# Kernel tuning notes

Measured on AMD Instinct MI355X. Metric: run time of the kernel, lower is better.

Reference implementation:

```python
import jax, jax.numpy as jnp
import numpy as np
from jax import lax

V_TH = 1.0
ALPHA = 2.0  # ATan surrogate alpha
EPS = 1e-5

@jax.custom_vjp
def heaviside(x):
    return (x >= 0).astype(x.dtype)

def _hv_fwd(x):
    return (x >= 0).astype(x.dtype), x

def _hv_bwd(x, g):
    # ATan surrogate: alpha/2 / (1 + (pi/2 * alpha * x)^2)
    return (g * (ALPHA / 2.0) / (1.0 + (jnp.pi / 2.0 * ALPHA * x) ** 2),)

heaviside.defvjp(_hv_fwd, _hv_bwd)

def if_multistep(x_seq):
    # IF neuron, v_threshold=1.0, v_reset=0.0 (hard reset), over leading time dim
    def step(v, x):
        h = v + x
        s = heaviside(h - V_TH)
        v_new = h * (1.0 - s)  # hard reset to 0
        return v_new, s
    _, spikes = lax.scan(step, jnp.zeros_like(x_seq[0]), x_seq)
    return spikes

def conv2d(x, w):
    return lax.conv_general_dilated(x, w, (1, 1), 'SAME',
                                    dimension_numbers=('NCHW', 'OIHW', 'NCHW'))

def bn(x, g, b, m, v):
    inv = g / jnp.sqrt(v + EPS)
    return x * inv[None, :, None, None] + (b - m * inv)[None, :, None, None]

def maxpool2(x):  # [N,C,H,W] -> [N,C,H/2,W/2]
    return lax.reduce_window(x, -jnp.inf, lax.max, (1, 1, 2, 2), (1, 1, 2, 2), 'VALID')

def setup_inputs() -> dict:
    key = jax.random.key(0)
    ks = jax.random.split(key, 5)
    B = 128
    return {
        'x': jax.random.normal(ks[0], (B, 1, 28, 28), jnp.float32),
        'conv1_w': jax.random.normal(ks[1], (128, 1, 3, 3), jnp.float32),
        'bn1_g': jnp.ones((128,), jnp.float32),
        'bn1_b': jnp.zeros((128,), jnp.float32),
        'bn1_m': jnp.zeros((128,), jnp.float32),
        'bn1_v': jnp.ones((128,), jnp.float32),
        'conv2_w': jax.random.normal(ks[2], (128, 128, 3, 3), jnp.float32) * 0.05,
        'bn2_g': jnp.ones((128,), jnp.float32),
        'bn2_b': jnp.zeros((128,), jnp.float32),
        'bn2_m': jnp.zeros((128,), jnp.float32),
        'bn2_v': jnp.ones((128,), jnp.float32),
        'fc1_w': jax.random.normal(ks[3], (2048, 6272), jnp.float32) * 0.02,
        'fc2_w': jax.random.normal(ks[4], (10, 2048), jnp.float32) * 0.02,
        'T': 8,
    }

def reference(x, conv1_w, bn1_g, bn1_b, bn1_m, bn1_v, conv2_w, bn2_g, bn2_b, bn2_m, bn2_v, fc1_w, fc2_w, T):
    B = x.shape[0]
    # static conv (shared across timesteps)
    y = bn(conv2d(x, conv1_w), bn1_g, bn1_b, bn1_m, bn1_v)  # [B,128,28,28]
    x_seq = jnp.broadcast_to(y[None], (T,) + y.shape)        # [T,B,128,28,28]
    s1 = if_multistep(x_seq)
    # maxpool -> conv -> bn, per timestep (fold T into batch)
    z = s1.reshape(T * B, 128, 28, 28)
    z = maxpool2(z)                                           # [TB,128,14,14]
    z = bn(conv2d(z, conv2_w), bn2_g, bn2_b, bn2_m, bn2_v)
    s2 = if_multistep(z.reshape(T, B, 128, 14, 14))
    z = maxpool2(s2.reshape(T * B, 128, 14, 14))              # [TB,128,7,7]
    z = z.reshape(T, B, 128 * 7 * 7)                          # flatten
    h = jnp.einsum('tbi,oi->tbo', z, fc1_w)                   # [T,B,2048]
    s3 = if_multistep(h)
    o = jnp.einsum('tbi,oi->tbo', s3, fc2_w)                  # [T,B,10]
    s4 = if_multistep(o)
    return s4.mean(0)                                         # [B,10]
```

## Files before the change

### kernel.cpp

```cpp
#include <hip/hip_runtime.h>
#include <stdint.h>

typedef unsigned int u32;
typedef unsigned long long u64;
typedef unsigned char u8;
typedef signed char s8;
typedef int v4i __attribute__((ext_vector_type(4)));
typedef int v16i __attribute__((ext_vector_type(16)));

#define TSTEPS 8
#define BATCH 128
#define CH 128
#define NPIX1 784
#define NPIX2 196
#define TB 1024
#define FC1_OUT 2048
#define FC1_IN 6272
#define FC2_OUT 10

#define W2_DIGITS 4
#define W2_SCALE 4294967296.0
#define W2_INVSCALE 2.3283064365386963e-10

#define FC1_DIGITS 4
#define FC1_KB 196
#define FC1_SCALE 8589934592.0
#define FC1_INVSCALE 1.1641532182693481e-10

#define P1S_PITCH 25216

typedef __attribute__((address_space(3))) u32 lds_u32;
typedef const __attribute__((address_space(1))) u32 glb_u32;
#define GLOAD16(G, L) __builtin_amdgcn_global_load_lds((glb_u32*)(G), (lds_u32*)(L), 16, 0, 0)

__global__ __launch_bounds__(256) void k1_conv1_if_pool(
    const float* __restrict__ x, const float* __restrict__ w1,
    const float* __restrict__ g1, const float* __restrict__ b1,
    const float* __restrict__ m1, const float* __restrict__ v1,
    u8* __restrict__ p1s)
{
    int bx = blockIdx.x;
    int b = bx >> 2, cg = bx & 3;
    int tid = threadIdx.x;

    __shared__ float xs[NPIX1];
    __shared__ double wt[32][13];
    __shared__ u8 sbits[NPIX1 * 32];

    for (int i = tid; i < NPIX1; i += 256) xs[i] = x[(size_t)b * NPIX1 + i];
    if (tid < 32) {
        int co = cg * 32 + tid;
#pragma unroll
        for (int k = 0; k < 9; ++k) wt[tid][k] = (double)w1[co * 9 + k];
        double inv = (double)g1[co] / sqrt((double)v1[co] + 1e-5);
        wt[tid][9]  = inv;
        wt[tid][10] = (double)b1[co] - (double)m1[co] * inv;
    }
    __syncthreads();

    for (int i = tid; i < NPIX1 * 32; i += 256) {
        int co = i & 31, p = i >> 5;
        int y = p / 28, xx = p - y * 28;
        double acc = 0.0;
#pragma unroll
        for (int dy = 0; dy < 3; ++dy) {
            int iy = y + dy - 1;
#pragma unroll
            for (int dx = 0; dx < 3; ++dx) {
                int ix = xx + dx - 1;
                if (iy >= 0 && iy < 28 && ix >= 0 && ix < 28)
                    acc += (double)xs[iy * 28 + ix] * wt[co][dy * 3 + dx];
            }
        }
        double yv = acc * wt[co][9] + wt[co][10];
        double v = 0.0; u32 byte = 0;
#pragma unroll
        for (int t = 0; t < 8; ++t) {
            double h = v + yv;
            int s = (h >= 1.0);
            byte |= (u32)s << t;
            v = s ? 0.0 : h;
        }
        sbits[p * 32 + co] = (u8)byte;
    }
    __syncthreads();

    for (int i = tid; i < NPIX2 * 32; i += 256) {
        int co = i & 31, p14 = i >> 5;
        int y14 = p14 / 14, x14 = p14 - y14 * 14;
        int p0 = (2 * y14) * 28 + 2 * x14;
        u8 pv = sbits[p0 * 32 + co] | sbits[(p0 + 1) * 32 + co]
              | sbits[(p0 + 28) * 32 + co] | sbits[(p0 + 29) * 32 + co];
        int off = (p14 * 128 + cg * 32 + co) ^ ((p14 & 7) << 4);
#pragma unroll
        for (int t = 0; t < 8; ++t)
            p1s[(size_t)(t * BATCH + b) * P1S_PITCH + off] = (u8)((pv >> t) & 1);
    }
}

__global__ __launch_bounds__(256) void k2w_quant(
    const float* __restrict__ w2, s8* __restrict__ Bt)
{
    int g = blockIdx.x * 256 + threadIdx.x;
    if (g >= CH * CH) return;
    int co = g >> 7, ci = g & 127;
    int ks = ci >> 5, rem = ci & 31, half = rem >> 4, bp = rem & 15;
    int l = (co & 31) | (half << 5);
    int Nt = co >> 5;
#pragma unroll
    for (int k = 0; k < 9; ++k) {
        double wd = (double)w2[(size_t)g * 9 + k] * W2_SCALE;
        long r = (long)llrint(wd);
#pragma unroll
        for (int d = 0; d < W2_DIGITS; ++d) {
            int dg = (int)(((r + 128) & 255) - 128);
            r = (r - (long)dg) >> 8;
            Bt[((size_t)(((d * 9 + k) * 4 + ks) * 4 + Nt)) * 1024 + l * 16 + bp] = (s8)dg;
        }
    }
}

__global__ __launch_bounds__(512, 2) void k2_conv2_if_pool(
    const u8* __restrict__ p1s, const s8* __restrict__ Bt,
    const float* __restrict__ g2, const float* __restrict__ bb2,
    const float* __restrict__ m2, const float* __restrict__ v2,
    u8* __restrict__ z2)
{
    int bx = blockIdx.x;
    int b = bx >> 2, cq = bx & 3;

    int tid = threadIdx.x;
    int lane = tid & 63;
    int lane32 = lane & 31;
    int khalf = (lane >> 5) << 4;
    int w = __builtin_amdgcn_readfirstlane(tid >> 6);
    int rhi = (lane >> 5) * 4;

    __shared__ u8 sp[P1S_PITCH];
    __shared__ u8 bbuf[2][36864];
    __shared__ u8 sbuf[NPIX2 * 32];

    if (tid < 8) *(uint4*)(sp + 196 * 128 + tid * 16) = make_uint4(0u, 0u, 0u, 0u);

    int co = cq * 32 + lane32;
    double binv  = (double)g2[co] / sqrt((double)v2[co] + 1e-5);
    double bbeta = (double)bb2[co] - (double)m2[co] * binv;

    int p = w * 32 + lane32;
    int valid = (p < NPIX2);
    int pe = valid ? p : 0;
    int py = pe / 14, px = pe - py * 14;
    int pixb[9], psw[9];
#pragma unroll
    for (int tap = 0; tap < 9; ++tap) {
        int dy = tap / 3 - 1, dx = tap - (tap / 3) * 3 - 1;
        int ny = py + dy, nx = px + dx;
        int ok = valid & (ny >= 0) & (ny < 14) & (nx >= 0) & (nx < 14);
        int pixn = ok ? (ny * 14 + nx) : 196;
        pixb[tap] = pixn * 128;
        psw[tap]  = (pixn & 7) << 4;
    }

    auto stageB = [&](int ks, int bufsel) {
#pragma unroll
        for (int i = 0; i < 5; ++i) {
            int f = w + i * 8;
            if (f < 36) {
                GLOAD16(Bt + ((size_t)((f * 4 + ks) * 4 + cq)) * 1024 + lane * 16,
                        bbuf[bufsel] + f * 1024);
            }
        }
    };

    {
        const u8* s0 = p1s + (size_t)b * P1S_PITCH;
        for (int i = tid; i < 1568; i += 512) GLOAD16(s0 + i * 16, sp + i * 16);
        stageB(0, 0);
    }
    __syncthreads();

    double vst[16];
#pragma unroll
    for (int r = 0; r < 16; ++r) vst[r] = 0.0;

#pragma unroll 1
    for (int t = 0; t < TSTEPS; ++t) {
        v16i acc[4];
#pragma unroll
        for (int d = 0; d < 4; ++d)
#pragma unroll
            for (int r = 0; r < 16; ++r) acc[d][r] = 0;

#pragma unroll 1
        for (int ks = 0; ks < 4; ++ks) {
            int cur = ks & 1;
            stageB((ks + 1) & 3, cur ^ 1);

            v4i A[9];
#pragma unroll
            for (int tap = 0; tap < 9; ++tap)
                A[tap] = *(const v4i*)(sp + pixb[tap] + ((ks * 32 + khalf) ^ psw[tap]));

            const u8* bbp = bbuf[cur];
#pragma unroll
            for (int d = 0; d < 4; ++d) {
#pragma unroll
                for (int tap = 0; tap < 9; ++tap) {
                    v4i B = *(const v4i*)(bbp + (d * 9 + tap) * 1024 + lane * 16);
                    acc[d] = __builtin_amdgcn_mfma_i32_32x32x32_i8(A[tap], B, acc[d], 0, 0, 0);
                }
            }
            __syncthreads();
        }

        if (t + 1 < TSTEPS) {
            const u8* sn = p1s + (size_t)((t + 1) * BATCH + b) * P1S_PITCH;
            for (int i = tid; i < 1568; i += 512) GLOAD16(sn + i * 16, sp + i * 16);
        }

#pragma unroll
        for (int r = 0; r < 16; ++r) {
            long carry = ((long)acc[3][r] << 24) + ((long)acc[2][r] << 16)
                       + ((long)acc[1][r] << 8) + (long)acc[0][r];
            int pix = w * 32 + (r & 3) + 8 * (r >> 2) + rhi;
            double hin = (double)carry * W2_INVSCALE * binv + bbeta;
            double hv = vst[r] + hin;
            int s = (hv >= 1.0);
            vst[r] = s ? 0.0 : hv;
            if (pix < NPIX2) sbuf[pix * 32 + lane32] = (u8)s;
        }
        __syncthreads();

        int tb = t * BATCH + b;
        for (int j = tid; j < 49 * 32; j += 512) {
            int w49 = j >> 5, c32 = j & 31;
            int wy = w49 / 7, wx = w49 - wy * 7;
            int p0 = (2 * wy) * 14 + 2 * wx;
            u8 s = sbuf[p0 * 32 + c32] | sbuf[(p0 + 1) * 32 + c32]
                 | sbuf[(p0 + 14) * 32 + c32] | sbuf[(p0 + 15) * 32 + c32];
            int i2 = (cq * 32 + c32) * 49 + w49;
            z2[((size_t)(i2 >> 5) * TB + tb) * 32 + (i2 & 31)] = s;
        }
        __syncthreads();
    }
}

__global__ __launch_bounds__(256) void k4w_quant(
    const float* __restrict__ fw, s8* __restrict__ Wd1)
{
    int g = blockIdx.x * 256 + threadIdx.x;
    if (g >= FC1_KB * FC1_OUT) return;
    int o = g & 2047, kb = g >> 11;

    u32 tmp[FC1_DIGITS][8];
#pragma unroll
    for (int d = 0; d < FC1_DIGITS; ++d)
#pragma unroll
        for (int q = 0; q < 8; ++q) tmp[d][q] = 0;

#pragma unroll
    for (int j = 0; j < 32; ++j) {
        double wd = (double)fw[(size_t)o * FC1_IN + kb * 32 + j] * FC1_SCALE;
        long r = (long)llrint(wd);
#pragma unroll
        for (int d = 0; d < FC1_DIGITS; ++d) {
            int dg = (int)(((r + 128) & 255) - 128);
            r = (r - (long)dg) >> 8;
            tmp[d][j >> 2] |= (u32)(dg & 255) << ((j & 3) * 8);
        }
    }
#pragma unroll
    for (int d = 0; d < FC1_DIGITS; ++d) {
        u32* dst = (u32*)(Wd1 + (((size_t)d * FC1_KB + kb) * FC1_OUT + o) * 32);
        *(uint4*)dst       = make_uint4(tmp[d][0], tmp[d][1], tmp[d][2], tmp[d][3]);
        *(uint4*)(dst + 4) = make_uint4(tmp[d][4], tmp[d][5], tmp[d][6], tmp[d][7]);
    }
}

__global__ __launch_bounds__(512, 2) void k4_fc1_i8(
    const u8* __restrict__ z2, const s8* __restrict__ Wd1,
    int* __restrict__ Hpart)
{
    __shared__ u8 stg[2 * 24576];

    int bx = blockIdx.x;
    int ntd = bx & 31, mt = bx >> 5;
    int nt = ntd >> 2, d = ntd & 3;

    int tid = threadIdx.x;
    int lane = tid & 63, lane32 = lane & 31;
    int half16 = (lane >> 5) << 4;
    int wv = __builtin_amdgcn_readfirstlane(tid >> 6);
    int wm = wv >> 2, wn = wv & 3;

    int tb0 = mt * 128, o0 = nt * 256;

    v16i acc00, acc01, acc10, acc11;
#pragma unroll
    for (int r = 0; r < 16; ++r) { acc00[r] = 0; acc01[r] = 0; acc10[r] = 0; acc11[r] = 0; }

    auto stage = [&](int q, int buf) {
        int kbg0 = q * 2;
        for (int i = wv; i < 24; i += 8) {
            if (i < 8) {
                int kbr = i >> 2, sub = i & 3;
                GLOAD16(z2 + ((size_t)(kbg0 + kbr) * TB + tb0 + sub * 32 + lane32) * 32 + half16,
                        stg + buf * 24576 + i * 1024);
            } else {
                int j = i - 8;
                int kbr = j >> 3, osub = j & 7;
                GLOAD16(Wd1 + (((size_t)d * FC1_KB + kbg0 + kbr) * FC1_OUT + o0 + osub * 32 + lane32) * 32 + half16,
                        stg + buf * 24576 + 8192 + j * 1024);
            }
        }
    };

    stage(0, 0);
    __syncthreads();

#pragma unroll 1
    for (int q = 0; q < 98; ++q) {
        int buf = q & 1;
        if (q + 1 < 98) stage(q + 1, buf ^ 1);
        const u8* A_ = stg + buf * 24576;
        const u8* B_ = A_ + 8192;
#pragma unroll
        for (int kbr = 0; kbr < 2; ++kbr) {
            v4i A0 = *(const v4i*)(A_ + (kbr * 4 + wm * 2 + 0) * 1024 + lane * 16);
            v4i A1 = *(const v4i*)(A_ + (kbr * 4 + wm * 2 + 1) * 1024 + lane * 16);
            v4i B0 = *(const v4i*)(B_ + (kbr * 8 + wn * 2 + 0) * 1024 + lane * 16);
            v4i B1 = *(const v4i*)(B_ + (kbr * 8 + wn * 2 + 1) * 1024 + lane * 16);
            acc00 = __builtin_amdgcn_mfma_i32_32x32x32_i8(A0, B0, acc00, 0, 0, 0);
            acc01 = __builtin_amdgcn_mfma_i32_32x32x32_i8(A0, B1, acc01, 0, 0, 0);
            acc10 = __builtin_amdgcn_mfma_i32_32x32x32_i8(A1, B0, acc10, 0, 0, 0);
            acc11 = __builtin_amdgcn_mfma_i32_32x32x32_i8(A1, B1, acc11, 0, 0, 0);
        }
        __syncthreads();
    }

    int rhi = (lane >> 5) << 2;
    int* Hd = Hpart + (size_t)d * TB * FC1_OUT;
#pragma unroll
    for (int r = 0; r < 16; ++r) {
        int row = (r & 3) + 8 * (r >> 2) + rhi;
        size_t b0 = (size_t)(tb0 + wm * 64 + row) * FC1_OUT + o0 + wn * 64 + lane32;
        Hd[b0]                             = acc00[r];
        Hd[b0 + 32]                        = acc01[r];
        Hd[b0 + (size_t)32 * FC1_OUT]      = acc10[r];
        Hd[b0 + (size_t)32 * FC1_OUT + 32] = acc11[r];
    }
}

__global__ __launch_bounds__(256) void k5_if3(
    const int* __restrict__ Hpart, u8* __restrict__ s3)
{
    int g = blockIdx.x * 256 + threadIdx.x;
    int b = g >> 11;
    int o = g & 2047;
    double v = 0.0;
#pragma unroll
    for (int t = 0; t < 8; ++t) {
        size_t idx = (size_t)(t * BATCH + b) * FC1_OUT + o;
        long c = 0;
#pragma unroll
        for (int d = 0; d < FC1_DIGITS; ++d)
            c += ((long)Hpart[(size_t)d * TB * FC1_OUT + idx]) << (8 * d);
        double h = v + (double)c * FC1_INVSCALE;
        int s = (h >= 1.0);
        v = s ? 0.0 : h;
        s3[idx] = (u8)s;
    }
}

__global__ __launch_bounds__(256) void k6_fc2(
    const u8* __restrict__ s3, const float* __restrict__ fw2,
    double* __restrict__ h4)
{
    int tb = blockIdx.x;
    int tid = threadIdx.x;
    int w = tid >> 6, lane = tid & 63;
    __shared__ double red[4][16];

    double acc[10];
#pragma unroll
    for (int o = 0; o < 10; ++o) acc[o] = 0.0;

#pragma unroll
    for (int it = 0; it < 8; ++it) {
        int i = w * 512 + it * 64 + lane;
        double zd = (double)s3[(size_t)tb * FC1_OUT + i];
#pragma unroll
        for (int o = 0; o < 10; ++o)
            acc[o] += zd * (double)fw2[o * FC1_OUT + i];
    }
#pragma unroll
    for (int o = 0; o < 10; ++o) {
#pragma unroll
        for (int off = 32; off >= 1; off >>= 1)
            acc[o] += __shfl_down(acc[o], off);
    }
    if (lane == 0) {
#pragma unroll
        for (int o = 0; o < 10; ++o) red[w][o] = acc[o];
    }
    __syncthreads();
    if (tid < 10)
        h4[(size_t)tb * 16 + tid] = red[0][tid] + red[1][tid] + red[2][tid] + red[3][tid];
}

__global__ __launch_bounds__(256) void k7_if4_mean(
    const double* __restrict__ h4, float* __restrict__ out)
{
    int g = blockIdx.x * 256 + threadIdx.x;
    if (g >= BATCH * FC2_OUT) return;
    int b = g / 10;
    int o = g - b * 10;
    double v = 0.0; int cnt = 0;
#pragma unroll
    for (int t = 0; t < 8; ++t) {
        double h = v + h4[(size_t)(t * BATCH + b) * 16 + o];
        int s = (h >= 1.0);
        cnt += s;
        v = s ? 0.0 : h;
    }
    out[b * 10 + o] = (float)cnt * 0.125f;
}

extern "C" void kernel_launch(void* const* d_in, const int* in_sizes, int n_in,
                              void* d_out, int out_size, void* d_ws, size_t ws_size,
                              hipStream_t stream)
{
    const float* x   = (const float*)d_in[0];
    const float* w1  = (const float*)d_in[1];
    const float* g1  = (const float*)d_in[2];
    const float* b1  = (const float*)d_in[3];
    const float* m1  = (const float*)d_in[4];
    const float* v1  = (const float*)d_in[5];
    const float* w2  = (const float*)d_in[6];
    const float* g2  = (const float*)d_in[7];
    const float* b2  = (const float*)d_in[8];
    const float* m2  = (const float*)d_in[9];
    const float* v2  = (const float*)d_in[10];
    const float* fw1 = (const float*)d_in[11];
    const float* fw2 = (const float*)d_in[12];
    float* out = (float*)d_out;

    char* ws = (char*)d_ws;
    size_t off = 0;
    auto alloc = [&](size_t sz) { size_t o = off; off = (off + sz + 255) & ~(size_t)255; return o; };

    size_t o_p1 = alloc((size_t)TB * P1S_PITCH);
    size_t o_z  = alloc((size_t)TB * FC1_IN);
    size_t o_s3 = alloc((size_t)TB * FC1_OUT);
    size_t o_h4 = alloc((size_t)TB * 16 * 8);
    size_t o_wd = alloc((size_t)W2_DIGITS * 9 * CH * CH);
    size_t o_w1 = alloc((size_t)FC1_DIGITS * FC1_KB * FC1_OUT * 32);
    size_t o_hp = alloc((size_t)FC1_DIGITS * TB * FC1_OUT * 4);
    (void)ws_size;

    u8*     p1s    = (u8*)(ws + o_p1);
    u8*     z2     = (u8*)(ws + o_z);
    u8*     s3     = (u8*)(ws + o_s3);
    double* h4     = (double*)(ws + o_h4);
    s8*     Bt     = (s8*)(ws + o_wd);
    s8*     Wd1    = (s8*)(ws + o_w1);
    int*    Hpart  = (int*)(ws + o_hp);

    k2w_quant<<<dim3((CH * CH + 255) / 256), dim3(256), 0, stream>>>(w2, Bt);

    k4w_quant<<<dim3((FC1_KB * FC1_OUT + 255) / 256), dim3(256), 0, stream>>>(
        fw1, Wd1);

    k1_conv1_if_pool<<<dim3(512), dim3(256), 0, stream>>>(
        x, w1, g1, b1, m1, v1, p1s);

    k2_conv2_if_pool<<<dim3(512), dim3(512), 0, stream>>>(
        p1s, Bt, g2, b2, m2, v2, z2);

    k4_fc1_i8<<<dim3(256), dim3(512), 0, stream>>>(z2, Wd1, Hpart);

    k5_if3<<<dim3(BATCH * FC1_OUT / 256), dim3(256), 0, stream>>>(Hpart, s3);

    k6_fc2<<<dim3(TB), dim3(256), 0, stream>>>(s3, fw2, h4);

    k7_if4_mean<<<dim3((BATCH * FC2_OUT + 255) / 256), dim3(256), 0, stream>>>(h4, out);
}
```

Measured before the change: 341.0 us.

## Fuse IF3, FC2 and IF4-mean into one per-batch kernel

Replaces the three tail kernels with one kernel per batch sample that reconstructs FC1 outputs, runs the IF neuron into shared memory, computes FC2 per timestep and the final IF plus mean. It removes two launches and the global round-trips of the s3 and h4 intermediates. In exchange only 128 blocks run, reducing parallelism and memory-level parallelism for reading the large Hpart buffer.

Result: slower. 366.3 us (+7.4%).

```diff
diff --git a/kernel.cpp b/kernel.cpp
--- a/kernel.cpp
+++ b/kernel.cpp
@@ -351,79 +351,72 @@
     }
 }
 
-__global__ __launch_bounds__(256) void k5_if3(
-    const int* __restrict__ Hpart, u8* __restrict__ s3)
-{
-    int g = blockIdx.x * 256 + threadIdx.x;
-    int b = g >> 11;
-    int o = g & 2047;
-    double v = 0.0;
-#pragma unroll
-    for (int t = 0; t < 8; ++t) {
-        size_t idx = (size_t)(t * BATCH + b) * FC1_OUT + o;
-        long c = 0;
-#pragma unroll
-        for (int d = 0; d < FC1_DIGITS; ++d)
-            c += ((long)Hpart[(size_t)d * TB * FC1_OUT + idx]) << (8 * d);
-        double h = v + (double)c * FC1_INVSCALE;
-        int s = (h >= 1.0);
-        v = s ? 0.0 : h;
-        s3[idx] = (u8)s;
-    }
-}
-
-__global__ __launch_bounds__(256) void k6_fc2(
-    const u8* __restrict__ s3, const float* __restrict__ fw2,
-    double* __restrict__ h4)
-{
-    int tb = blockIdx.x;
+__global__ __launch_bounds__(256) void k5_fused(
+    const int* __restrict__ Hpart, const float* __restrict__ fw2,
+    float* __restrict__ out)
+{
+    int b = blockIdx.x;
     int tid = threadIdx.x;
     int w = tid >> 6, lane = tid & 63;
-    __shared__ double red[4][16];
-
-    double acc[10];
-#pragma unroll
-    for (int o = 0; o < 10; ++o) acc[o] = 0.0;
-
-#pragma unroll
-    for (int it = 0; it < 8; ++it) {
-        int i = w * 512 + it * 64 + lane;
-        double zd = (double)s3[(size_t)tb * FC1_OUT + i];
-#pragma unroll
-        for (int o = 0; o < 10; ++o)
-            acc[o] += zd * (double)fw2[o * FC1_OUT + i];
-    }
-#pragma unroll
-    for (int o = 0; o < 10; ++o) {
-#pragma unroll
-        for (int off = 32; off >= 1; off >>= 1)
-            acc[o] += __shfl_down(acc[o], off);
-    }
-    if (lane == 0) {
-#pragma unroll
-        for (int o = 0; o < 10; ++o) red[w][o] = acc[o];
-    }
-    __syncthreads();
-    if (tid < 10)
-        h4[(size_t)tb * 16 + tid] = red[0][tid] + red[1][tid] + red[2][tid] + red[3][tid];
-}
-
-__global__ __launch_bounds__(256) void k7_if4_mean(
-    const double* __restrict__ h4, float* __restrict__ out)
-{
-    int g = blockIdx.x * 256 + threadIdx.x;
-    if (g >= BATCH * FC2_OUT) return;
-    int b = g / 10;
-    int o = g - b * 10;
-    double v = 0.0; int cnt = 0;
-#pragma unroll
-    for (int t = 0; t < 8; ++t) {
-        double h = v + h4[(size_t)(t * BATCH + b) * 16 + o];
-        int s = (h >= 1.0);
-        cnt += s;
-        v = s ? 0.0 : h;
-    }
-    out[b * 10 + o] = (float)cnt * 0.125f;
+
+    __shared__ u8 s3l[TSTEPS][FC1_OUT];
+    __shared__ double red[TSTEPS][16];
+
+#pragma unroll
+    for (int q = 0; q < 8; ++q) {
+        int o = tid + q * 256;
+        double v = 0.0;
+#pragma unroll
+        for (int t = 0; t < TSTEPS; ++t) {
+            size_t idx = (size_t)(t * BATCH + b) * FC1_OUT + o;
+            long c = 0;
+#pragma unroll
+            for (int d = 0; d < FC1_DIGITS; ++d)
+                c += ((long)Hpart[(size_t)d * TB * FC1_OUT + idx]) << (8 * d);
+            double h = v + (double)c * FC1_INVSCALE;
+            int s = (h >= 1.0);
+            v = s ? 0.0 : h;
+            s3l[t][o] = (u8)s;
+        }
+    }
+    __syncthreads();
+
+#pragma unroll
+    for (int half = 0; half < 2; ++half) {
+        int t = w + half * 4;
+        double acc[10];
+#pragma unroll
+        for (int o = 0; o < 10; ++o) acc[o] = 0.0;
+        for (int i = lane; i < FC1_OUT; i += 64) {
+            double zd = (double)s3l[t][i];
+#pragma unroll
+            for (int o = 0; o < 10; ++o)
+                acc[o] += zd * (double)fw2[o * FC1_OUT + i];
+        }
+#pragma unroll
+        for (int o = 0; o < 10; ++o) {
+#pragma unroll
+            for (int off = 32; off >= 1; off >>= 1)
+                acc[o] += __shfl_down(acc[o], off);
+        }
+        if (lane == 0) {
+#pragma unroll
+            for (int o = 0; o < 10; ++o) red[t][o] = acc[o];
+        }
+    }
+    __syncthreads();
+
+    if (tid < 10) {
+        double v = 0.0; int cnt = 0;
+#pragma unroll
+        for (int t = 0; t < TSTEPS; ++t) {
+            double h = v + red[t][tid];
+            int s = (h >= 1.0);
+            cnt += s;
+            v = s ? 0.0 : h;
+        }
+        out[b * 10 + tid] = (float)cnt * 0.125f;
+    }
 }
 
 extern "C" void kernel_launch(void* const* d_in, const int* in_sizes, int n_in,
@@ -451,8 +444,6 @@
 
     size_t o_p1 = alloc((size_t)TB * P1S_PITCH);
     size_t o_z  = alloc((size_t)TB * FC1_IN);
-    size_t o_s3 = alloc((size_t)TB * FC1_OUT);
-    size_t o_h4 = alloc((size_t)TB * 16 * 8);
     size_t o_wd = alloc((size_t)W2_DIGITS * 9 * CH * CH);
     size_t o_w1 = alloc((size_t)FC1_DIGITS * FC1_KB * FC1_OUT * 32);
     size_t o_hp = alloc((size_t)FC1_DIGITS * TB * FC1_OUT * 4);
@@ -460,8 +451,6 @@
 
     u8*     p1s    = (u8*)(ws + o_p1);
     u8*     z2     = (u8*)(ws + o_z);
-    u8*     s3     = (u8*)(ws + o_s3);
-    double* h4     = (double*)(ws + o_h4);
     s8*     Bt     = (s8*)(ws + o_wd);
     s8*     Wd1    = (s8*)(ws + o_w1);
     int*    Hpart  = (int*)(ws + o_hp);
@@ -479,9 +468,5 @@
 
     k4_fc1_i8<<<dim3(256), dim3(512), 0, stream>>>(z2, Wd1, Hpart);
 
-    k5_if3<<<dim3(BATCH * FC1_OUT / 256), dim3(256), 0, stream>>>(Hpart, s3);
-
-    k6_fc2<<<dim3(TB), dim3(256), 0, stream>>>(s3, fw2, h4);
-
-    k7_if4_mean<<<dim3((BATCH * FC2_OUT + 255) / 256), dim3(256), 0, stream>>>(h4, out);
-}
+    k5_fused<<<dim3(BATCH), dim3(256), 0, stream>>>(Hpart, fw2, out);
+}
```

## Process two timesteps per pass in conv2 kernel to share weight fragments

Applied to the files above, without the earlier changes.

The conv2+IF+pool kernel now handles timesteps in pairs. It double-buffers the pooled spike input and the spike output buffer in shared memory, so each weight fragment loaded from LDS feeds two MFMAs, one per timestep. This halves weight staging and B-fragment LDS traffic, and halves the block barriers per timestep. In exchange the accumulator register footprint doubles and LDS use grows, which may pressure occupancy or cause spills. The IF membrane update still runs sequentially, first timestep then second, so semantics are preserved.

Result: faster. 325.2 us (-4.7%).

```diff
diff --git a/kernel.cpp b/kernel.cpp
--- a/kernel.cpp
+++ b/kernel.cpp
@@ -136,11 +136,14 @@
     int w = __builtin_amdgcn_readfirstlane(tid >> 6);
     int rhi = (lane >> 5) * 4;
 
-    __shared__ u8 sp[P1S_PITCH];
+    __shared__ u8 sp[2][P1S_PITCH];
     __shared__ u8 bbuf[2][36864];
-    __shared__ u8 sbuf[NPIX2 * 32];
-
-    if (tid < 8) *(uint4*)(sp + 196 * 128 + tid * 16) = make_uint4(0u, 0u, 0u, 0u);
+    __shared__ u8 sbuf[2][NPIX2 * 32];
+
+    if (tid < 16) {
+        int pl = tid >> 3;
+        *(uint4*)(sp[pl] + 196 * 128 + (tid & 7) * 16) = make_uint4(0u, 0u, 0u, 0u);
+    }
 
     int co = cq * 32 + lane32;
     double binv  = (double)g2[co] / sqrt((double)v2[co] + 1e-5);
@@ -150,15 +153,14 @@
     int valid = (p < NPIX2);
     int pe = valid ? p : 0;
     int py = pe / 14, px = pe - py * 14;
-    int pixb[9], psw[9];
+    int comb[9];
 #pragma unroll
     for (int tap = 0; tap < 9; ++tap) {
         int dy = tap / 3 - 1, dx = tap - (tap / 3) * 3 - 1;
         int ny = py + dy, nx = px + dx;
         int ok = valid & (ny >= 0) & (ny < 14) & (nx >= 0) & (nx < 14);
         int pixn = ok ? (ny * 14 + nx) : 196;
-        pixb[tap] = pixn * 128;
-        psw[tap]  = (pixn & 7) << 4;
+        comb[tap] = pixn * 128 + ((pixn & 7) << 4);
     }
 
     auto stageB = [&](int ks, int bufsel) {
@@ -174,7 +176,9 @@
 
     {
         const u8* s0 = p1s + (size_t)b * P1S_PITCH;
-        for (int i = tid; i < 1568; i += 512) GLOAD16(s0 + i * 16, sp + i * 16);
+        const u8* s1 = p1s + (size_t)(BATCH + b) * P1S_PITCH;
+        for (int i = tid; i < 1568; i += 512) GLOAD16(s0 + i * 16, sp[0] + i * 16);
+        for (int i = tid; i < 1568; i += 512) GLOAD16(s1 + i * 16, sp[1] + i * 16);
         stageB(0, 0);
     }
     __syncthreads();
@@ -184,61 +188,69 @@
     for (int r = 0; r < 16; ++r) vst[r] = 0.0;
 
 #pragma unroll 1
-    for (int t = 0; t < TSTEPS; ++t) {
-        v16i acc[4];
-#pragma unroll
-        for (int d = 0; d < 4; ++d)
-#pragma unroll
-            for (int r = 0; r < 16; ++r) acc[d][r] = 0;
+    for (int tg = 0; tg < 4; ++tg) {
+        v16i acc[2][4];
+#pragma unroll
+        for (int h = 0; h < 2; ++h)
+#pragma unroll
+            for (int d = 0; d < 4; ++d)
+#pragma unroll
+                for (int r = 0; r < 16; ++r) acc[h][d][r] = 0;
 
 #pragma unroll 1
         for (int ks = 0; ks < 4; ++ks) {
             int cur = ks & 1;
             stageB((ks + 1) & 3, cur ^ 1);
 
-            v4i A[9];
-#pragma unroll
-            for (int tap = 0; tap < 9; ++tap)
-                A[tap] = *(const v4i*)(sp + pixb[tap] + ((ks * 32 + khalf) ^ psw[tap]));
-
+            int K = ks * 32 + khalf;
             const u8* bbp = bbuf[cur];
 #pragma unroll
-            for (int d = 0; d < 4; ++d) {
-#pragma unroll
-                for (int tap = 0; tap < 9; ++tap) {
+            for (int tap = 0; tap < 9; ++tap) {
+                v4i A0 = *(const v4i*)(sp[0] + (comb[tap] ^ K));
+                v4i A1 = *(const v4i*)(sp[1] + (comb[tap] ^ K));
+#pragma unroll
+                for (int d = 0; d < 4; ++d) {
                     v4i B = *(const v4i*)(bbp + (d * 9 + tap) * 1024 + lane * 16);
-                    acc[d] = __builtin_amdgcn_mfma_i32_32x32x32_i8(A[tap], B, acc[d], 0, 0, 0);
+                    acc[0][d] = __builtin_amdgcn_mfma_i32_32x32x32_i8(A0, B, acc[0][d], 0, 0, 0);
+                    acc[1][d] = __builtin_amdgcn_mfma_i32_32x32x32_i8(A1, B, acc[1][d], 0, 0, 0);
                 }
             }
             __syncthreads();
         }
 
-        if (t + 1 < TSTEPS) {
-            const u8* sn = p1s + (size_t)((t + 1) * BATCH + b) * P1S_PITCH;
-            for (int i = tid; i < 1568; i += 512) GLOAD16(sn + i * 16, sp + i * 16);
-        }
-
-#pragma unroll
-        for (int r = 0; r < 16; ++r) {
-            long carry = ((long)acc[3][r] << 24) + ((long)acc[2][r] << 16)
-                       + ((long)acc[1][r] << 8) + (long)acc[0][r];
-            int pix = w * 32 + (r & 3) + 8 * (r >> 2) + rhi;
-            double hin = (double)carry * W2_INVSCALE * binv + bbeta;
-            double hv = vst[r] + hin;
-            int s = (hv >= 1.0);
-            vst[r] = s ? 0.0 : hv;
-            if (pix < NPIX2) sbuf[pix * 32 + lane32] = (u8)s;
+        if (tg + 1 < 4) {
+            const u8* sn0 = p1s + (size_t)((2 * tg + 2) * BATCH + b) * P1S_PITCH;
+            const u8* sn1 = p1s + (size_t)((2 * tg + 3) * BATCH + b) * P1S_PITCH;
+            for (int i = tid; i < 1568; i += 512) GLOAD16(sn0 + i * 16, sp[0] + i * 16);
+            for (int i = tid; i < 1568; i += 512) GLOAD16(sn1 + i * 16, sp[1] + i * 16);
+        }
+
+#pragma unroll
+        for (int h = 0; h < 2; ++h) {
+#pragma unroll
+            for (int r = 0; r < 16; ++r) {
+                long carry = ((long)acc[h][3][r] << 24) + ((long)acc[h][2][r] << 16)
+                           + ((long)acc[h][1][r] << 8) + (long)acc[h][0][r];
+                int pix = w * 32 + (r & 3) + 8 * (r >> 2) + rhi;
+                double hin = (double)carry * W2_INVSCALE * binv + bbeta;
+                double hv = vst[r] + hin;
+                int s = (hv >= 1.0);
+                vst[r] = s ? 0.0 : hv;
+                if (pix < NPIX2) sbuf[h][pix * 32 + lane32] = (u8)s;
+            }
         }
         __syncthreads();
 
-        int tb = t * BATCH + b;
-        for (int j = tid; j < 49 * 32; j += 512) {
-            int w49 = j >> 5, c32 = j & 31;
+        for (int j = tid; j < 2 * 49 * 32; j += 512) {
+            int h = (j >= 49 * 32);
+            int jj = j - h * (49 * 32);
+            int w49 = jj >> 5, c32 = jj & 31;
             int wy = w49 / 7, wx = w49 - wy * 7;
             int p0 = (2 * wy) * 14 + 2 * wx;
-            u8 s = sbuf[p0 * 32 + c32] | sbuf[(p0 + 1) * 32 + c32]
-                 | sbuf[(p0 + 14) * 32 + c32] | sbuf[(p0 + 15) * 32 + c32];
+            u8 s = sbuf[h][p0 * 32 + c32] | sbuf[h][(p0 + 1) * 32 + c32]
+                 | sbuf[h][(p0 + 14) * 32 + c32] | sbuf[h][(p0 + 15) * 32 + c32];
             int i2 = (cq * 32 + c32) * 49 + w49;
+            int tb = (2 * tg + h) * BATCH + b;
             z2[((size_t)(i2 >> 5) * TB + tb) * 32 + (i2 & 31)] = s;
         }
         __syncthreads();
```
